# Performance work log

Measured on AMD Instinct MI355X. Metric: run time of the kernel, lower is better.

The kernel has to match this reference:

```python
import jax, jax.numpy as jnp
import numpy as np

N, IN_DIM, OUT_DIM, NUM_EXPERTS, TOP_K = 8192, 1024, 1024, 8, 2


def setup_inputs() -> dict:
    key = jax.random.key(0)
    ks = jax.random.split(key, 5)
    s_in = 1.0 / np.sqrt(IN_DIM)
    x = jax.random.normal(ks[0], (N, IN_DIM), dtype=jnp.float32)
    # per-expert Linear weights: [E, in, out] (torch Linear weight is [out,in]; we store transposed)
    W = jax.random.uniform(ks[1], (NUM_EXPERTS, IN_DIM, OUT_DIM), jnp.float32, -s_in, s_in)
    b = jax.random.uniform(ks[2], (NUM_EXPERTS, OUT_DIM), jnp.float32, -s_in, s_in)
    Wg = jax.random.uniform(ks[3], (IN_DIM, NUM_EXPERTS), jnp.float32, -s_in, s_in)
    bg = jax.random.uniform(ks[4], (NUM_EXPERTS,), jnp.float32, -s_in, s_in)
    return {"x": x, "W": W, "b": b, "Wg": Wg, "bg": bg}


def reference(x, W, b, Wg, bg):
    # gating scores [N, E]
    scores = x @ Wg + bg
    # top-k mask
    _, top_idx = jax.lax.top_k(scores, TOP_K)  # [N, k]
    mask = jnp.zeros_like(scores).at[jnp.arange(x.shape[0])[:, None], top_idx].set(1.0)
    masked = jnp.where(mask == 0, -jnp.inf, scores)
    gating_weights = jax.nn.softmax(masked, axis=-1)  # [N, E]
    # all-expert linear: [N, E, out]
    expert_outputs = jnp.einsum('ni,eio->neo', x, W) + b
    # weighted combine over experts
    return jnp.einsum('ne,neo->no', gating_weights, expert_outputs)
```

## Files before the change

### kernel.cpp

```cpp
#include <hip/hip_runtime.h>

#define N_TOK 8192
#define IN_DIM 1024
#define OUT_DIM 1024
#define NE 8
#define TILE_SH 12288

typedef short short8 __attribute__((ext_vector_type(8)));
typedef float f32x4 __attribute__((ext_vector_type(4)));
typedef ushort ushort4v __attribute__((ext_vector_type(4)));

__device__ __forceinline__ ushort f2bf(float f) {
    union { float f; unsigned u; } v; v.f = f;
    unsigned u = v.u;
    unsigned r = (u + 0x7fffu + ((u >> 16) & 1u)) >> 16;
    return (ushort)r;
}

__device__ __forceinline__ float bf2f(short s) {
    union { unsigned u; float f; } v;
    v.u = ((unsigned)(unsigned short)s) << 16;
    return v.f;
}

__device__ __forceinline__ void gl_lds16(const short* g, short* l) {
    __builtin_amdgcn_global_load_lds(
        (const __attribute__((address_space(1))) unsigned int*)g,
        (__attribute__((address_space(3))) unsigned int*)l, 16, 0, 0);
}

__global__ __launch_bounds__(256) void gate_convert(const float* __restrict__ x,
                                                    const float* __restrict__ Wg,
                                                    const float* __restrict__ bg,
                                                    short* __restrict__ xb,
                                                    unsigned* __restrict__ choice,
                                                    float2* __restrict__ wts) {
    int wid = threadIdx.x >> 6, lane = threadIdx.x & 63;
    int tok = blockIdx.x * 4 + wid;
    const float* xr = x + (size_t)tok * IN_DIM;
    short* xbr = xb + (size_t)tok * IN_DIM;
    float acc[8];
    #pragma unroll
    for (int e = 0; e < 8; ++e) acc[e] = 0.f;
    #pragma unroll
    for (int it = 0; it < 4; ++it) {
        int j = it * 256 + lane * 4;
        float4 v = *(const float4*)(xr + j);
        ushort4v o;
        o[0] = f2bf(v.x); o[1] = f2bf(v.y); o[2] = f2bf(v.z); o[3] = f2bf(v.w);
        *(ushort4v*)(xbr + j) = o;
        #pragma unroll
        for (int r = 0; r < 4; ++r) {
            float xv = (r == 0) ? v.x : (r == 1) ? v.y : (r == 2) ? v.z : v.w;
            float4 wa = *(const float4*)(Wg + (size_t)(j + r) * 8);
            float4 wb = *(const float4*)(Wg + (size_t)(j + r) * 8 + 4);
            acc[0] += xv * wa.x; acc[1] += xv * wa.y;
            acc[2] += xv * wa.z; acc[3] += xv * wa.w;
            acc[4] += xv * wb.x; acc[5] += xv * wb.y;
            acc[6] += xv * wb.z; acc[7] += xv * wb.w;
        }
    }
    #pragma unroll
    for (int e = 0; e < 8; ++e)
        #pragma unroll
        for (int off = 32; off; off >>= 1)
            acc[e] += __shfl_xor(acc[e], off, 64);
    if (lane == 0) {
        float s[8];
        #pragma unroll
        for (int e = 0; e < 8; ++e) s[e] = acc[e] + bg[e];
        int i0 = 0;
        #pragma unroll
        for (int e = 1; e < 8; ++e) if (s[e] > s[i0]) i0 = e;
        int i1 = (i0 == 0) ? 1 : 0;
        #pragma unroll
        for (int e = 0; e < 8; ++e) if (e != i0 && s[e] > s[i1]) i1 = e;
        float e0 = 1.f, e1 = __expf(s[i1] - s[i0]);
        float inv = 1.f / (e0 + e1);
        choice[tok] = (unsigned)i0 | ((unsigned)i1 << 8);
        wts[tok] = make_float2(e0 * inv, e1 * inv);
    }
}

__global__ __launch_bounds__(1024) void bucket(const unsigned* __restrict__ choice,
                                               const float2* __restrict__ wts,
                                               int* __restrict__ counts,
                                               int* __restrict__ entries,
                                               int* __restrict__ inv0,
                                               int* __restrict__ inv1) {
    int e = blockIdx.x;
    int t = threadIdx.x;
    int wid = t >> 6, lane = t & 63;
    __shared__ int wsum[16];
    int base = 0;
    for (int chunk = 0; chunk < 8; ++chunk) {
        int tok = chunk * 1024 + t;
        unsigned c = choice[tok];
        int which = ((int)(c & 255u) == e) ? 0 : (((int)((c >> 8) & 255u) == e) ? 1 : -1);
        unsigned long long m = __ballot(which >= 0);
        if (lane == 0) wsum[wid] = __popcll(m);
        __syncthreads();
        int woff = base;
        #pragma unroll
        for (int i = 0; i < 16; ++i) if (i < wid) woff += wsum[i];
        int tot = 0;
        #pragma unroll
        for (int i = 0; i < 16; ++i) tot += wsum[i];
        if (which >= 0) {
            int rank = __popcll(m & ((1ull << lane) - 1ull));
            int idx = woff + rank;
            entries[e * N_TOK + idx] = tok;
            if (which == 0) inv0[tok] = idx; else inv1[tok] = idx;
        }
        base += tot;
        __syncthreads();
    }
    if (t == 0) counts[e] = base;
}

__global__ __launch_bounds__(256) void transpose_w(const float* __restrict__ W,
                                                   short* __restrict__ wt) {
    int e = blockIdx.z, kt = blockIdx.y, nt = blockIdx.x;
    __shared__ ushort tile[32][33];
    int t = threadIdx.x;
    int r = t >> 3;
    int c4 = (t & 7) * 4;
    const float4 v = *(const float4*)(W + (((size_t)e * 1024 + kt * 32 + r) * 1024) + nt * 32 + c4);
    tile[c4 + 0][r] = f2bf(v.x);
    tile[c4 + 1][r] = f2bf(v.y);
    tile[c4 + 2][r] = f2bf(v.z);
    tile[c4 + 3][r] = f2bf(v.w);
    __syncthreads();
    int n = t >> 3, kq = (t & 7) * 4;
    ushort4v o;
    o[0] = tile[n][kq + 0]; o[1] = tile[n][kq + 1];
    o[2] = tile[n][kq + 2]; o[3] = tile[n][kq + 3];
    *(ushort4v*)(wt + (((size_t)e * 1024 + nt * 32 + n) * 1024) + kt * 32 + kq) = o;
}

__global__ __launch_bounds__(256, 2) void moe_gemm(const short* __restrict__ xb,
                                                   const short* __restrict__ wt,
                                                   const float* __restrict__ bias,
                                                   const int* __restrict__ counts,
                                                   const int* __restrict__ entries,
                                                   short* __restrict__ ys) {
    int lin = blockIdx.x;
    int e = lin & 7;
    int inner = lin >> 3;
    int ct = inner & 3, rt = inner >> 2;
    int cnt = counts[e];
    if (rt * 128 >= cnt) return;
    int rows = min(128, cnt - rt * 128);
    int base_e = 0;
    #pragma unroll
    for (int i = 0; i < NE; ++i) base_e += (i < e) ? counts[i] : 0;

    __shared__ __align__(16) short lds[3 * TILE_SH];
    __shared__ int tok_sh[128];

    int t = threadIdx.x, wid = t >> 6, lane = t & 63;
    int ebase = e * N_TOK + rt * 128;
    if (t < 128) tok_sh[t] = (t < rows) ? entries[ebase + t] : entries[ebase];
    __syncthreads();

    int chunkoff = (((t & 3) ^ ((t >> 2) & 3)) * 8);
    const short* asrc0 = xb + (size_t)tok_sh[t >> 2] * IN_DIM + chunkoff;
    const short* asrc1 = xb + (size_t)tok_sh[64 + (t >> 2)] * IN_DIM + chunkoff;
    const short* bsrc0 = wt + ((size_t)e * OUT_DIM + ct * 256 + (t >> 2)) * IN_DIM + chunkoff;
    const short* bsrc1 = bsrc0 + (size_t)64 * IN_DIM;
    const short* bsrc2 = bsrc0 + (size_t)128 * IN_DIM;
    const short* bsrc3 = bsrc0 + (size_t)192 * IN_DIM;
    int dst8 = t * 8;

    int wr = wid >> 1, wc = wid & 1;
    int frow = lane & 15, fslot = lane >> 4;
    int rslot = (fslot ^ (frow & 3)) * 8;
    int aoff[4], boff[8];
    #pragma unroll
    for (int mi = 0; mi < 4; ++mi) aoff[mi] = (wr * 64 + mi * 16 + frow) * 32 + rslot;
    #pragma unroll
    for (int ni = 0; ni < 8; ++ni) boff[ni] = (wc * 128 + ni * 16 + frow) * 32 + rslot;

    f32x4 acc[4][8];
    #pragma unroll
    for (int mi = 0; mi < 4; ++mi)
        #pragma unroll
        for (int ni = 0; ni < 8; ++ni) acc[mi][ni] = (f32x4)(0.0f);

#define STAGE(BUF, KT)                                                        \
    {                                                                         \
        short* nb = lds + (BUF) * TILE_SH;                                    \
        int nk = (KT) * 32;                                                   \
        gl_lds16(asrc0 + nk, nb + dst8);                                      \
        gl_lds16(asrc1 + nk, nb + 2048 + dst8);                               \
        gl_lds16(bsrc0 + nk, nb + 4096 + dst8);                               \
        gl_lds16(bsrc1 + nk, nb + 6144 + dst8);                               \
        gl_lds16(bsrc2 + nk, nb + 8192 + dst8);                               \
        gl_lds16(bsrc3 + nk, nb + 10240 + dst8);                              \
    }

#define GITER(CUR, NXT, KTN, VN, DO_STAGE)                                    \
    {                                                                         \
        asm volatile("s_waitcnt vmcnt(" VN ")" ::: "memory");                 \
        __builtin_amdgcn_s_barrier();                                         \
        __builtin_amdgcn_sched_barrier(0);                                    \
        const short* Ab = lds + (CUR) * TILE_SH;                              \
        const short* Bb = Ab + 4096;                                          \
        short8 afv[4], bfv[8];                                                \
        _Pragma("unroll")                                                     \
        for (int mi = 0; mi < 4; ++mi) afv[mi] = *(const short8*)(Ab + aoff[mi]); \
        _Pragma("unroll")                                                     \
        for (int ni = 0; ni < 8; ++ni) bfv[ni] = *(const short8*)(Bb + boff[ni]); \
        if (DO_STAGE) STAGE(NXT, KTN);                                        \
        __builtin_amdgcn_s_setprio(1);                                        \
        _Pragma("unroll")                                                     \
        for (int mi = 0; mi < 4; ++mi)                                        \
            _Pragma("unroll")                                                 \
            for (int ni = 0; ni < 8; ++ni)                                    \
                acc[mi][ni] = __builtin_amdgcn_mfma_f32_16x16x32_bf16(        \
                    afv[mi], bfv[ni], acc[mi][ni], 0, 0, 0);                  \
        __builtin_amdgcn_s_setprio(0);                                        \
    }

    STAGE(0, 0);
    STAGE(1, 1);

    for (int kt = 0; kt < 30; kt += 3) {
        GITER(0, 2, kt + 2, "6", 1);
        GITER(1, 0, kt + 3, "6", 1);
        GITER(2, 1, kt + 4, "6", 1);
    }
    GITER(0, 0, 0, "6", 0);
    GITER(1, 0, 0, "0", 0);

#undef GITER
#undef STAGE

    __syncthreads();
    short* ep = lds;
    const float* be = bias + (size_t)e * OUT_DIM;
    #pragma unroll
    for (int ni = 0; ni < 8; ++ni) {
        int col = wc * 128 + ni * 16 + frow;
        float bv = be[ct * 256 + col];
        #pragma unroll
        for (int mi = 0; mi < 4; ++mi) {
            int rb_ = wr * 64 + mi * 16 + fslot * 4;
            #pragma unroll
            for (int r = 0; r < 4; ++r)
                ep[(rb_ + r) * 264 + col] = (short)f2bf(acc[mi][ni][r] + bv);
        }
    }
    __syncthreads();
    #pragma unroll
    for (int k = 0; k < 16; ++k) {
        int f = t + k * 256;
        int row = f >> 5, cw = f & 31;
        if (row < rows) {
            short8 v = *(const short8*)(ep + row * 264 + cw * 8);
            *(short8*)(ys + ((size_t)(base_e + rt * 128 + row)) * OUT_DIM
                       + ct * 256 + cw * 8) = v;
        }
    }
}

__global__ __launch_bounds__(256) void combine(const short* __restrict__ ys,
                                               const unsigned* __restrict__ choice,
                                               const float2* __restrict__ wts,
                                               const int* __restrict__ inv0,
                                               const int* __restrict__ inv1,
                                               const int* __restrict__ counts,
                                               float* __restrict__ out) {
    __shared__ int bases[8];
    if (threadIdx.x < 8) {
        int s = 0;
        #pragma unroll
        for (int i = 0; i < 8; ++i) s += (i < (int)threadIdx.x) ? counts[i] : 0;
        bases[threadIdx.x] = s;
    }
    __syncthreads();
    int tok = blockIdx.x * 2 + (threadIdx.x >> 7);
    int c8 = (threadIdx.x & 127) * 8;
    unsigned ch = choice[tok];
    float2 w = wts[tok];
    int p0 = bases[ch & 255u] + inv0[tok];
    int p1 = bases[(ch >> 8) & 255u] + inv1[tok];
    short8 a = *(const short8*)(ys + (size_t)p0 * OUT_DIM + c8);
    short8 b = *(const short8*)(ys + (size_t)p1 * OUT_DIM + c8);
    float* op = out + (size_t)tok * OUT_DIM + c8;
    float4 o0, o1;
    o0.x = w.x * bf2f(a[0]) + w.y * bf2f(b[0]);
    o0.y = w.x * bf2f(a[1]) + w.y * bf2f(b[1]);
    o0.z = w.x * bf2f(a[2]) + w.y * bf2f(b[2]);
    o0.w = w.x * bf2f(a[3]) + w.y * bf2f(b[3]);
    o1.x = w.x * bf2f(a[4]) + w.y * bf2f(b[4]);
    o1.y = w.x * bf2f(a[5]) + w.y * bf2f(b[5]);
    o1.z = w.x * bf2f(a[6]) + w.y * bf2f(b[6]);
    o1.w = w.x * bf2f(a[7]) + w.y * bf2f(b[7]);
    *(float4*)op = o0;
    *(float4*)(op + 4) = o1;
}

extern "C" void kernel_launch(void* const* d_in, const int* in_sizes, int n_in,
                              void* d_out, int out_size, void* d_ws, size_t ws_size,
                              hipStream_t stream) {
    const float* x  = (const float*)d_in[0];
    const float* W  = (const float*)d_in[1];
    const float* b  = (const float*)d_in[2];
    const float* Wg = (const float*)d_in[3];
    const float* bg = (const float*)d_in[4];
    float* out = (float*)d_out;

    char* ws = (char*)d_ws;
    short* xb        = (short*)(ws);
    short* wt        = (short*)(ws + 16777216);
    unsigned* choice = (unsigned*)(ws + 33554432);
    float2* wts      = (float2*)(ws + 33587200);
    int* inv0        = (int*)(ws + 33652736);
    int* inv1        = (int*)(ws + 33685504);
    int* entries     = (int*)(ws + 33718272);
    int* counts      = (int*)(ws + 34242560);
    short* ys        = (short*)(ws + 34242624);

    gate_convert<<<2048, 256, 0, stream>>>(x, Wg, bg, xb, choice, wts);
    bucket<<<8, 1024, 0, stream>>>(choice, wts, counts, entries, inv0, inv1);
    transpose_w<<<dim3(32, 32, 8), 256, 0, stream>>>(W, wt);
    moe_gemm<<<2048, 256, 0, stream>>>(xb, wt, b, counts, entries, ys);
    combine<<<4096, 256, 0, stream>>>(ys, choice, wts, inv0, inv1, counts, out);
}
```

Baseline: 123.2 us.

## Split MFMA k-step into two half-phases with interleaved staging and wider LDS swizzle

Each k-iteration of the grouped expert GEMM is split into two halves. Each half loads four B fragments from LDS, issues half of the global-to-LDS loads for the next stage, and runs a 4x4 block of MFMAs, with an extra barrier between the halves. The LDS XOR swizzle also mixes in one more row bit on both the write and read sides to cut bank conflicts. The intent is to spread memory traffic across the MFMA work and lower peak register use, at the cost of an extra barrier per iteration and a vmcnt wait count that may no longer match the split load groups.

```diff
diff --git a/kernel.cpp b/kernel.cpp
--- a/kernel.cpp
+++ b/kernel.cpp
@@ -163,7 +163,7 @@
     if (t < 128) tok_sh[t] = (t < rows) ? entries[ebase + t] : entries[ebase];
     __syncthreads();
 
-    int chunkoff = (((t & 3) ^ ((t >> 2) & 3)) * 8);
+    int chunkoff = (((t & 3) ^ ((t >> 2) & 3) ^ ((t >> 4) & 3)) * 8);
     const short* asrc0 = xb + (size_t)tok_sh[t >> 2] * IN_DIM + chunkoff;
     const short* asrc1 = xb + (size_t)tok_sh[64 + (t >> 2)] * IN_DIM + chunkoff;
     const short* bsrc0 = wt + ((size_t)e * OUT_DIM + ct * 256 + (t >> 2)) * IN_DIM + chunkoff;
@@ -174,7 +174,7 @@
 
     int wr = wid >> 1, wc = wid & 1;
     int frow = lane & 15, fslot = lane >> 4;
-    int rslot = (fslot ^ (frow & 3)) * 8;
+    int rslot = ((fslot ^ (frow & 3) ^ ((frow >> 2) & 3)) * 8);
     int aoff[4], boff[8];
     #pragma unroll
     for (int mi = 0; mi < 4; ++mi) aoff[mi] = (wr * 64 + mi * 16 + frow) * 32 + rslot;
@@ -187,13 +187,18 @@
         #pragma unroll
         for (int ni = 0; ni < 8; ++ni) acc[mi][ni] = (f32x4)(0.0f);
 
-#define STAGE(BUF, KT)                                                        \
+#define STAGE_A(BUF, KT)                                                      \
     {                                                                         \
         short* nb = lds + (BUF) * TILE_SH;                                    \
         int nk = (KT) * 32;                                                   \
         gl_lds16(asrc0 + nk, nb + dst8);                                      \
         gl_lds16(asrc1 + nk, nb + 2048 + dst8);                               \
         gl_lds16(bsrc0 + nk, nb + 4096 + dst8);                               \
+    }
+#define STAGE_B(BUF, KT)                                                      \
+    {                                                                         \
+        short* nb = lds + (BUF) * TILE_SH;                                    \
+        int nk = (KT) * 32;                                                   \
         gl_lds16(bsrc1 + nk, nb + 6144 + dst8);                               \
         gl_lds16(bsrc2 + nk, nb + 8192 + dst8);                               \
         gl_lds16(bsrc3 + nk, nb + 10240 + dst8);                              \
@@ -206,24 +211,38 @@
         __builtin_amdgcn_sched_barrier(0);                                    \
         const short* Ab = lds + (CUR) * TILE_SH;                              \
         const short* Bb = Ab + 4096;                                          \
-        short8 afv[4], bfv[8];                                                \
+        short8 afv[4], bfv[4];                                                \
         _Pragma("unroll")                                                     \
         for (int mi = 0; mi < 4; ++mi) afv[mi] = *(const short8*)(Ab + aoff[mi]); \
         _Pragma("unroll")                                                     \
-        for (int ni = 0; ni < 8; ++ni) bfv[ni] = *(const short8*)(Bb + boff[ni]); \
-        if (DO_STAGE) STAGE(NXT, KTN);                                        \
+        for (int ni = 0; ni < 4; ++ni) bfv[ni] = *(const short8*)(Bb + boff[ni]); \
+        if (DO_STAGE) STAGE_A(NXT, KTN);                                      \
         __builtin_amdgcn_s_setprio(1);                                        \
         _Pragma("unroll")                                                     \
         for (int mi = 0; mi < 4; ++mi)                                        \
             _Pragma("unroll")                                                 \
-            for (int ni = 0; ni < 8; ++ni)                                    \
+            for (int ni = 0; ni < 4; ++ni)                                    \
                 acc[mi][ni] = __builtin_amdgcn_mfma_f32_16x16x32_bf16(        \
                     afv[mi], bfv[ni], acc[mi][ni], 0, 0, 0);                  \
         __builtin_amdgcn_s_setprio(0);                                        \
-    }
-
-    STAGE(0, 0);
-    STAGE(1, 1);
+        __builtin_amdgcn_s_barrier();                                         \
+        __builtin_amdgcn_sched_barrier(0);                                    \
+        short8 bgv[4];                                                        \
+        _Pragma("unroll")                                                     \
+        for (int ni = 0; ni < 4; ++ni) bgv[ni] = *(const short8*)(Bb + boff[ni + 4]); \
+        if (DO_STAGE) STAGE_B(NXT, KTN);                                      \
+        __builtin_amdgcn_s_setprio(1);                                        \
+        _Pragma("unroll")                                                     \
+        for (int mi = 0; mi < 4; ++mi)                                        \
+            _Pragma("unroll")                                                 \
+            for (int ni = 0; ni < 4; ++ni)                                    \
+                acc[mi][ni + 4] = __builtin_amdgcn_mfma_f32_16x16x32_bf16(    \
+                    afv[mi], bgv[ni], acc[mi][ni + 4], 0, 0, 0);              \
+        __builtin_amdgcn_s_setprio(0);                                        \
+    }
+
+    STAGE_A(0, 0); STAGE_B(0, 0);
+    STAGE_A(1, 1); STAGE_B(1, 1);
 
     for (int kt = 0; kt < 30; kt += 3) {
         GITER(0, 2, kt + 2, "6", 1);
@@ -234,7 +253,8 @@
     GITER(1, 0, 0, "0", 0);
 
 #undef GITER
-#undef STAGE
+#undef STAGE_A
+#undef STAGE_B
 
     __syncthreads();
     short* ep = lds;
```

Result: slower. 126.4 us (+2.6%).

## Enlarge MoE GEMM tile to 256x256 with 512-thread blocks and phased epilogue

Applied to the files above, without the earlier changes.

The grouped expert GEMM now uses 512-thread blocks computing 256-row by 256-column tiles instead of 128x256. Each of the 8 waves holds 8x4 MFMA accumulators, and the LDS swizzle gains an extra XOR term. The larger tile is meant to raise reuse of the staged A and B data and cut global loads per FLOP. The epilogue now writes through LDS in four 64-row phases so it fits in the triple-buffered 96KB LDS. In exchange, more rows are wasted padding per expert, fewer blocks are launched, and register pressure rises.

```diff
diff --git a/kernel.cpp b/kernel.cpp
--- a/kernel.cpp
+++ b/kernel.cpp
@@ -4,7 +4,7 @@
 #define IN_DIM 1024
 #define OUT_DIM 1024
 #define NE 8
-#define TILE_SH 12288
+#define TSH 16384
 
 typedef short short8 __attribute__((ext_vector_type(8)));
 typedef float f32x4 __attribute__((ext_vector_type(4)));
@@ -83,7 +83,6 @@
 }
 
 __global__ __launch_bounds__(1024) void bucket(const unsigned* __restrict__ choice,
-                                               const float2* __restrict__ wts,
                                                int* __restrict__ counts,
                                                int* __restrict__ entries,
                                                int* __restrict__ inv0,
@@ -138,7 +137,7 @@
     *(ushort4v*)(wt + (((size_t)e * 1024 + nt * 32 + n) * 1024) + kt * 32 + kq) = o;
 }
 
-__global__ __launch_bounds__(256, 2) void moe_gemm(const short* __restrict__ xb,
+__global__ __launch_bounds__(512, 2) void moe_gemm(const short* __restrict__ xb,
                                                    const short* __restrict__ wt,
                                                    const float* __restrict__ bias,
                                                    const int* __restrict__ counts,
@@ -147,56 +146,54 @@
     int lin = blockIdx.x;
     int e = lin & 7;
     int inner = lin >> 3;
-    int ct = inner & 3, rt = inner >> 2;
+    int rt = inner >> 2, ct = inner & 3;
     int cnt = counts[e];
-    if (rt * 128 >= cnt) return;
-    int rows = min(128, cnt - rt * 128);
+    if (rt * 256 >= cnt) return;
+    int rows = min(256, cnt - rt * 256);
     int base_e = 0;
     #pragma unroll
     for (int i = 0; i < NE; ++i) base_e += (i < e) ? counts[i] : 0;
 
-    __shared__ __align__(16) short lds[3 * TILE_SH];
-    __shared__ int tok_sh[128];
+    __shared__ __align__(16) short lds[3 * TSH];
+    __shared__ int tok_sh[256];
 
     int t = threadIdx.x, wid = t >> 6, lane = t & 63;
-    int ebase = e * N_TOK + rt * 128;
-    if (t < 128) tok_sh[t] = (t < rows) ? entries[ebase + t] : entries[ebase];
+    int ebase = e * N_TOK + rt * 256;
+    if (t < 256) tok_sh[t] = (t < rows) ? entries[ebase + t] : entries[ebase];
     __syncthreads();
 
-    int chunkoff = (((t & 3) ^ ((t >> 2) & 3)) * 8);
-    const short* asrc0 = xb + (size_t)tok_sh[t >> 2] * IN_DIM + chunkoff;
-    const short* asrc1 = xb + (size_t)tok_sh[64 + (t >> 2)] * IN_DIM + chunkoff;
-    const short* bsrc0 = wt + ((size_t)e * OUT_DIM + ct * 256 + (t >> 2)) * IN_DIM + chunkoff;
-    const short* bsrc1 = bsrc0 + (size_t)64 * IN_DIM;
-    const short* bsrc2 = bsrc0 + (size_t)128 * IN_DIM;
-    const short* bsrc3 = bsrc0 + (size_t)192 * IN_DIM;
-    int dst8 = t * 8;
-
-    int wr = wid >> 1, wc = wid & 1;
+    int r0 = t >> 2;
+    int chunkoff = (((t & 3) ^ (r0 & 3) ^ ((r0 >> 2) & 3)) * 8);
+    const short* asrc0 = xb + (size_t)tok_sh[r0] * IN_DIM + chunkoff;
+    const short* asrc1 = xb + (size_t)tok_sh[128 + r0] * IN_DIM + chunkoff;
+    const short* bsrc0 = wt + ((size_t)e * OUT_DIM + ct * 256 + r0) * IN_DIM + chunkoff;
+    const short* bsrc1 = bsrc0 + (size_t)128 * IN_DIM;
+    int dA0 = t * 8, dA1 = (t + 512) * 8;
+    int dB0 = 8192 + t * 8, dB1 = 8192 + (t + 512) * 8;
+
+    int wr = wid >> 2, wc = wid & 3;
     int frow = lane & 15, fslot = lane >> 4;
-    int rslot = (fslot ^ (frow & 3)) * 8;
-    int aoff[4], boff[8];
-    #pragma unroll
-    for (int mi = 0; mi < 4; ++mi) aoff[mi] = (wr * 64 + mi * 16 + frow) * 32 + rslot;
-    #pragma unroll
-    for (int ni = 0; ni < 8; ++ni) boff[ni] = (wc * 128 + ni * 16 + frow) * 32 + rslot;
-
-    f32x4 acc[4][8];
-    #pragma unroll
-    for (int mi = 0; mi < 4; ++mi)
-        #pragma unroll
-        for (int ni = 0; ni < 8; ++ni) acc[mi][ni] = (f32x4)(0.0f);
+    int rslot = ((fslot ^ (frow & 3) ^ ((frow >> 2) & 3)) * 8);
+    int aoff[8], boff[4];
+    #pragma unroll
+    for (int mi = 0; mi < 8; ++mi) aoff[mi] = (wr * 128 + mi * 16 + frow) * 32 + rslot;
+    #pragma unroll
+    for (int ni = 0; ni < 4; ++ni) boff[ni] = 8192 + (wc * 64 + ni * 16 + frow) * 32 + rslot;
+
+    f32x4 acc[8][4];
+    #pragma unroll
+    for (int mi = 0; mi < 8; ++mi)
+        #pragma unroll
+        for (int ni = 0; ni < 4; ++ni) acc[mi][ni] = (f32x4)(0.0f);
 
 #define STAGE(BUF, KT)                                                        \
     {                                                                         \
-        short* nb = lds + (BUF) * TILE_SH;                                    \
+        short* nb = lds + (BUF) * TSH;                                        \
         int nk = (KT) * 32;                                                   \
-        gl_lds16(asrc0 + nk, nb + dst8);                                      \
-        gl_lds16(asrc1 + nk, nb + 2048 + dst8);                               \
-        gl_lds16(bsrc0 + nk, nb + 4096 + dst8);                               \
-        gl_lds16(bsrc1 + nk, nb + 6144 + dst8);                               \
-        gl_lds16(bsrc2 + nk, nb + 8192 + dst8);                               \
-        gl_lds16(bsrc3 + nk, nb + 10240 + dst8);                              \
+        gl_lds16(asrc0 + nk, nb + dA0);                                       \
+        gl_lds16(asrc1 + nk, nb + dA1);                                       \
+        gl_lds16(bsrc0 + nk, nb + dB0);                                       \
+        gl_lds16(bsrc1 + nk, nb + dB1);                                       \
     }
 
 #define GITER(CUR, NXT, KTN, VN, DO_STAGE)                                    \
@@ -204,19 +201,18 @@
         asm volatile("s_waitcnt vmcnt(" VN ")" ::: "memory");                 \
         __builtin_amdgcn_s_barrier();                                         \
         __builtin_amdgcn_sched_barrier(0);                                    \
-        const short* Ab = lds + (CUR) * TILE_SH;                              \
-        const short* Bb = Ab + 4096;                                          \
-        short8 afv[4], bfv[8];                                                \
+        const short* Ab = lds + (CUR) * TSH;                                  \
+        short8 afv[8], bfv[4];                                                \
         _Pragma("unroll")                                                     \
-        for (int mi = 0; mi < 4; ++mi) afv[mi] = *(const short8*)(Ab + aoff[mi]); \
+        for (int mi = 0; mi < 8; ++mi) afv[mi] = *(const short8*)(Ab + aoff[mi]); \
         _Pragma("unroll")                                                     \
-        for (int ni = 0; ni < 8; ++ni) bfv[ni] = *(const short8*)(Bb + boff[ni]); \
+        for (int ni = 0; ni < 4; ++ni) bfv[ni] = *(const short8*)(Ab + boff[ni]); \
         if (DO_STAGE) STAGE(NXT, KTN);                                        \
         __builtin_amdgcn_s_setprio(1);                                        \
         _Pragma("unroll")                                                     \
-        for (int mi = 0; mi < 4; ++mi)                                        \
+        for (int mi = 0; mi < 8; ++mi)                                        \
             _Pragma("unroll")                                                 \
-            for (int ni = 0; ni < 8; ++ni)                                    \
+            for (int ni = 0; ni < 4; ++ni)                                    \
                 acc[mi][ni] = __builtin_amdgcn_mfma_f32_16x16x32_bf16(        \
                     afv[mi], bfv[ni], acc[mi][ni], 0, 0, 0);                  \
         __builtin_amdgcn_s_setprio(0);                                        \
@@ -226,40 +222,48 @@
     STAGE(1, 1);
 
     for (int kt = 0; kt < 30; kt += 3) {
-        GITER(0, 2, kt + 2, "6", 1);
-        GITER(1, 0, kt + 3, "6", 1);
-        GITER(2, 1, kt + 4, "6", 1);
-    }
-    GITER(0, 0, 0, "6", 0);
+        GITER(0, 2, kt + 2, "4", 1);
+        GITER(1, 0, kt + 3, "4", 1);
+        GITER(2, 1, kt + 4, "4", 1);
+    }
+    GITER(0, 0, 0, "4", 0);
     GITER(1, 0, 0, "0", 0);
 
 #undef GITER
 #undef STAGE
 
-    __syncthreads();
+    const float* be = bias + (size_t)e * OUT_DIM + ct * 256;
     short* ep = lds;
-    const float* be = bias + (size_t)e * OUT_DIM;
-    #pragma unroll
-    for (int ni = 0; ni < 8; ++ni) {
-        int col = wc * 128 + ni * 16 + frow;
-        float bv = be[ct * 256 + col];
-        #pragma unroll
-        for (int mi = 0; mi < 4; ++mi) {
-            int rb_ = wr * 64 + mi * 16 + fslot * 4;
+    #pragma unroll
+    for (int p = 0; p < 4; ++p) {
+        __syncthreads();
+        if (wr == (p >> 1)) {
+            int mib = (p & 1) * 4;
             #pragma unroll
-            for (int r = 0; r < 4; ++r)
-                ep[(rb_ + r) * 264 + col] = (short)f2bf(acc[mi][ni][r] + bv);
+            for (int mi2 = 0; mi2 < 4; ++mi2) {
+                int lrow = mi2 * 16 + fslot * 4;
+                #pragma unroll
+                for (int ni = 0; ni < 4; ++ni) {
+                    int col = wc * 64 + ni * 16 + frow;
+                    float bv = be[col];
+                    f32x4 a = acc[mib + mi2][ni];
+                    #pragma unroll
+                    for (int r = 0; r < 4; ++r)
+                        ep[(lrow + r) * 260 + col] = (short)f2bf(a[r] + bv);
+                }
+            }
         }
-    }
-    __syncthreads();
-    #pragma unroll
-    for (int k = 0; k < 16; ++k) {
-        int f = t + k * 256;
-        int row = f >> 5, cw = f & 31;
-        if (row < rows) {
-            short8 v = *(const short8*)(ep + row * 264 + cw * 8);
-            *(short8*)(ys + ((size_t)(base_e + rt * 128 + row)) * OUT_DIM
-                       + ct * 256 + cw * 8) = v;
+        __syncthreads();
+        #pragma unroll
+        for (int k = 0; k < 4; ++k) {
+            int u = t + k * 512;
+            int row = u >> 5, cw = u & 31;
+            int rl = p * 64 + row;
+            if (rl < rows) {
+                short8 v = *(const short8*)(ep + row * 260 + cw * 8);
+                *(short8*)(ys + (size_t)(base_e + rt * 256 + rl) * OUT_DIM
+                           + ct * 256 + cw * 8) = v;
+            }
         }
     }
 }
@@ -323,8 +327,8 @@
     short* ys        = (short*)(ws + 34242624);
 
     gate_convert<<<2048, 256, 0, stream>>>(x, Wg, bg, xb, choice, wts);
-    bucket<<<8, 1024, 0, stream>>>(choice, wts, counts, entries, inv0, inv1);
+    bucket<<<8, 1024, 0, stream>>>(choice, counts, entries, inv0, inv1);
     transpose_w<<<dim3(32, 32, 8), 256, 0, stream>>>(W, wt);
-    moe_gemm<<<2048, 256, 0, stream>>>(xb, wt, b, counts, entries, ys);
+    moe_gemm<<<1024, 512, 0, stream>>>(xb, wt, b, counts, entries, ys);
     combine<<<4096, 256, 0, stream>>>(ys, choice, wts, inv0, inv1, counts, out);
 }
```

Result: slower. 137.6 us (+11.7%).
